# Kernel optimization log

Measured on AMD Instinct MI355X. Metric: run time of the kernel, lower is better.

The kernel has to match this reference:

```python
import jax, jax.numpy as jnp
import numpy as np

VOX_X, VOX_Y, VOX_Z = 256, 256, 20   # ceil((pc_range[3:]-pc_range[:3]) / 0.4)
OUT_H, OUT_W, OUT_Z = 200, 200, 16   # hard-coded F.interpolate target in forward
C = 80                               # out_channels; sparse feat dim must match for concat
N_PTS = 200000
BS = 1
EPS = 1e-5


def _lin_interp(x, axis, out_size):
    """1D linear interp along `axis`, matching torch align_corners=False."""
    in_size = x.shape[axis]
    pos = (jnp.arange(out_size, dtype=jnp.float32) + 0.5) * (in_size / out_size) - 0.5
    pos = jnp.clip(pos, 0.0, in_size - 1)
    i0 = jnp.floor(pos).astype(jnp.int32)
    i1 = jnp.minimum(i0 + 1, in_size - 1)
    w = pos - i0.astype(jnp.float32)
    x0 = jnp.take(x, i0, axis=axis)
    x1 = jnp.take(x, i1, axis=axis)
    wshape = [1] * x.ndim
    wshape[axis] = out_size
    w = w.reshape(wshape)
    return x0 * (1.0 - w) + x1 * w


def setup_inputs() -> dict:
    key = jax.random.key(0)
    ks = jax.random.split(key, 8)
    bev_feats = jax.random.normal(ks[0], (BS, C, OUT_H, OUT_W, OUT_Z), dtype=jnp.float32)
    # coords: [batch_idx, x, y, z] with per-column valid ranges
    cb = jax.random.randint(ks[1], (N_PTS, 1), 0, BS, dtype=jnp.int32)
    cx = jax.random.randint(ks[2], (N_PTS, 1), 0, VOX_X, dtype=jnp.int32)
    cy = jax.random.randint(ks[3], (N_PTS, 1), 0, VOX_Y, dtype=jnp.int32)
    cz = jax.random.randint(ks[4], (N_PTS, 1), 0, VOX_Z, dtype=jnp.int32)
    coords = jnp.concatenate([cb, cx, cy, cz], axis=1)
    feats = jax.random.normal(ks[5], (N_PTS, C), dtype=jnp.float32)
    w_conv = jax.random.normal(ks[6], (C, 2 * C), dtype=jnp.float32) * (1.0 / np.sqrt(2 * C))
    b_conv = jnp.zeros((C,), dtype=jnp.float32)
    return {
        "bev_feats": bev_feats, "coords": coords, "feats": feats,
        "w_conv": w_conv, "b_conv": b_conv,
        "bn_gamma": jnp.ones((C,), jnp.float32), "bn_beta": jnp.zeros((C,), jnp.float32),
        "bn_mean": jnp.zeros((C,), jnp.float32), "bn_var": jnp.ones((C,), jnp.float32),
    }


def reference(bev_feats, coords, feats, w_conv, b_conv, bn_gamma, bn_beta, bn_mean, bn_var):
    bs = bev_feats.shape[0]
    voxel = jnp.zeros((bs, VOX_X, VOX_Y, VOX_Z, C), dtype=jnp.float32)
    voxel = voxel.at[coords[:, 0], coords[:, 1], coords[:, 2], coords[:, 3]].set(feats)
    # permute(0,4,2,1,3): (bs, X, Y, Z, C) -> (bs, C, Y, X, Z)
    prior = jnp.transpose(voxel, (0, 4, 2, 1, 3))
    # trilinear interpolate (256,256,20) -> (200,200,16), align_corners=False (separable)
    prior = _lin_interp(prior, 2, OUT_H)
    prior = _lin_interp(prior, 3, OUT_W)
    prior = _lin_interp(prior, 4, OUT_Z)
    # concat on channels -> 1x1x1 conv3d -> BN (eval stats) -> residual -> ReLU
    x = jnp.concatenate([bev_feats, prior], axis=1)  # (bs, 2C, H, W, Z)
    y = jnp.einsum('bchwz,oc->bohwz', x, w_conv) + b_conv[None, :, None, None, None]
    inv = bn_gamma * jax.lax.rsqrt(bn_var + EPS)
    y = y * inv[None, :, None, None, None] + (bn_beta - bn_mean * inv)[None, :, None, None, None]
    return jax.nn.relu(y + bev_feats)
```

## Files before the change

kernel.cpp:

```cpp
#include <hip/hip_runtime.h>
#include <hip/hip_bf16.h>

#define VXX 256
#define VYY 256
#define VZZ 20
#define NC  80
#define OH  200
#define OW  200
#define OZ  16
#define SPATIAL (OH*OW*OZ)
#define NVOX (VXX*VYY*VZZ)
#define EPSV 1e-5f
#define NS 64
#define RS 168
#define NWG (SPATIAL/NS)
#define X_FOOT 6
#define NCELL (2*X_FOOT*VZZ)
#define SLOTS 48
#define PSTR 72

typedef float  f32x4 __attribute__((ext_vector_type(4)));
typedef short  s16x8 __attribute__((ext_vector_type(8)));

__device__ __forceinline__ ushort f2bf(float f) {
    uint u = __builtin_bit_cast(uint, f);
    u += 0x7FFFu + ((u >> 16) & 1u);
    return (ushort)(u >> 16);
}

__device__ __forceinline__ void bar_lgkm() {
    asm volatile("s_waitcnt lgkmcnt(0)" ::: "memory");
    __builtin_amdgcn_s_barrier();
    asm volatile("" ::: "memory");
}

__global__ void scatter_k(const int* __restrict__ coords, int npts,
                          int* __restrict__ winner) {
    int i = blockIdx.x * 256 + threadIdx.x;
    if (i >= npts) return;
    int b = coords[i*4+0];
    int x = coords[i*4+1];
    int y = coords[i*4+2];
    int z = coords[i*4+3];
    int vi = ((b*VXX + x)*VYY + y)*VZZ + z;
    atomicMax(&winner[vi], i);
}

__global__ void setup_k(const float* __restrict__ wconv,
                        const float* __restrict__ bconv,
                        const float* __restrict__ gamma,
                        const float* __restrict__ beta,
                        const float* __restrict__ mean,
                        const float* __restrict__ var,
                        int4* __restrict__ winner4,
                        ushort* __restrict__ wfrag,
                        float2* __restrict__ bnss) {
    const int b = blockIdx.x, tid = threadIdx.x;
    if (b < 1280) {
        winner4[b*256 + tid] = make_int4(-1, -1, -1, -1);
    } else if (b < 1330) {
        int idx = (b - 1280)*256 + tid;
        int f   = idx >> 9;
        int rem = idx & 511;
        int l   = rem >> 3;
        int j   = rem & 7;
        int mt  = f / 5;
        int ks  = f - mt*5;
        int o   = mt*16 + (l & 15);
        int c   = ks*32 + (l >> 4)*8 + j;
        wfrag[idx] = f2bf(wconv[o*160 + c]);
    } else if (tid < NC) {
        float inv = gamma[tid] * rsqrtf(var[tid] + EPSV);
        bnss[tid] = make_float2(inv, bconv[tid]*inv + beta[tid] - mean[tid]*inv);
    }
}

__launch_bounds__(256, 3)
__global__ void fused_k(const float* __restrict__ bev,
                        const float* __restrict__ feats,
                        const int*  __restrict__ winner,
                        const ushort* __restrict__ wfrag,
                        const float2* __restrict__ bnss,
                        float* __restrict__ out) {
    __shared__ __align__(16) ushort x_lds[NS * RS];
    __shared__ __align__(16) ushort P_lds[NS * PSTR];
    __shared__ __align__(16) ushort Rt_lds[NC * PSTR];
    __shared__ int    idx_lds[NCELL];
    __shared__ int    slot_pi[SLOTS];
    __shared__ int    wavecnt[4];

    const int tid   = threadIdx.x;
    const int bid   = blockIdx.x;
    const int swzb  = (bid & 7) * (NWG/8) + (bid >> 3);
    const int sbase = swzb * NS;
    const int sl    = tid & 63;
    const int quarter = tid >> 6;
    const int wv    = quarter, lane = sl;

    const int h  = sbase / (OW * OZ);
    const int w0 = (sbase >> 4) % OW;
    float posy = (h + 0.5f) * ((float)VYY/(float)OH) - 0.5f;
    posy = fminf(fmaxf(posy, 0.f), (float)(VYY-1));
    const int   y0 = (int)posy;
    const int   y1 = min(y0+1, VYY-1);
    const float fy = posy - (float)y0;
    float posx0 = (w0 + 0.5f) * ((float)VXX/(float)OW) - 0.5f;
    posx0 = fminf(fmaxf(posx0, 0.f), (float)(VXX-1));
    const int xmin = (int)posx0;

    const int zq = sl & 15;
    const int wq = w0 + (sl >> 4);
    float posx = (wq + 0.5f) * ((float)VXX/(float)OW) - 0.5f;
    posx = fminf(fmaxf(posx, 0.f), (float)(VXX-1));
    const int   x0 = (int)posx;
    const int   x1 = min(x0+1, VXX-1);
    const float fxw = posx - (float)x0;
    float posz = (zq + 0.5f) * ((float)VZZ/(float)OZ) - 0.5f;
    posz = fminf(fmaxf(posz, 0.f), (float)(VZZ-1));
    const int   z0 = (int)posz;
    const int   z1 = min(z0+1, VZZ-1);
    const float fzw = posz - (float)z0;
    const int fx0 = x0 - xmin, fx1 = x1 - xmin;

    int pi = -1;
    if (tid < NCELL) {
        int fz  = tid % VZZ;
        int fx  = (tid / VZZ) % X_FOOT;
        int fyc = tid / (VZZ * X_FOOT);
        int xx  = min(xmin + fx, VXX-1);
        int yy  = fyc ? y1 : y0;
        pi = winner[(xx*VYY + yy)*VZZ + fz];
    }
    __builtin_amdgcn_sched_barrier(0);

    const int S = sbase + sl;
    float bvv[20];
    #pragma unroll
    for (int j = 0; j < 20; ++j)
        bvv[j] = bev[(quarter*20 + j)*SPATIAL + S];
    __builtin_amdgcn_sched_barrier(0);

    {
        uint* pz = (uint*)P_lds;
        #pragma unroll
        for (int i = 0; i < 9; ++i) pz[tid + i*256] = 0;
    }

    unsigned long long bm = __ballot(pi >= 0);
    if (lane == 0) wavecnt[wv] = __popcll(bm);
    bar_lgkm();
    int base = 0, nstot = 0;
    #pragma unroll
    for (int w2 = 0; w2 < 4; ++w2) {
        int c2 = wavecnt[w2];
        if (w2 < wv) base += c2;
        nstot += c2;
    }
    if (tid < NCELL) {
        int v = -1;
        if (pi >= 0) {
            int slot = base + __popcll(bm & ((1ull << lane) - 1ull));
            if (slot < SLOTS) { slot_pi[slot] = pi; v = slot; }
            else v = -(pi + 2);
        }
        idx_lds[tid] = v;
    }
    bar_lgkm();
    const int nst = min(nstot, SLOTS);

    const float4* feats4 = (const float4*)feats;
    const int myslot = tid >> 2, part = tid & 3;
    const bool rowact = (myslot < nst);
    float4 rbuf[5];
    if (rowact) {
        const float4* p = feats4 + slot_pi[myslot]*20 + part*5;
        #pragma unroll
        for (int q = 0; q < 5; ++q) rbuf[q] = p[q];
    }

    {
        const int ky = quarter >> 1, kx = quarter & 1;
        const float ywp = ky ? fy : 1.f - fy;
        const bool xdup = (fx1 == fx0);
        if (!(xdup && kx)) {
            const int   xf = kx ? fx1 : fx0;
            const float xw = xdup ? 1.f : (kx ? fxw : 1.f - fxw);
            #pragma unroll
            for (int kz = 0; kz < 2; ++kz) {
                int cell = (ky*X_FOOT + xf)*VZZ + (kz ? z1 : z0);
                int v = idx_lds[cell];
                if (v >= 0)
                    P_lds[sl*PSTR + v] = f2bf(ywp * xw * (kz ? fzw : 1.f - fzw));
            }
        }
    }

    #pragma unroll
    for (int j5 = 0; j5 < 5; ++j5) {
        ushort4 pk = make_ushort4(f2bf(bvv[j5*4+0]), f2bf(bvv[j5*4+1]),
                                  f2bf(bvv[j5*4+2]), f2bf(bvv[j5*4+3]));
        *(ushort4*)&x_lds[sl*RS + quarter*20 + j5*4] = pk;
    }

    {
        ushort vals[20];
        #pragma unroll
        for (int q = 0; q < 5; ++q) {
            vals[4*q+0] = rowact ? f2bf(rbuf[q].x) : (ushort)0;
            vals[4*q+1] = rowact ? f2bf(rbuf[q].y) : (ushort)0;
            vals[4*q+2] = rowact ? f2bf(rbuf[q].z) : (ushort)0;
            vals[4*q+3] = rowact ? f2bf(rbuf[q].w) : (ushort)0;
        }
        #pragma unroll
        for (int e = 0; e < 20; ++e)
            Rt_lds[(part*20 + e)*PSTR + myslot] = vals[e];
    }
    bar_lgkm();

    const int lrow = lane & 15, lgrp = lane >> 4;
    {
        const int prow = (wv*16 + lrow)*PSTR;
        s16x8 p0 = *(const s16x8*)&P_lds[prow +      lgrp*8];
        s16x8 p1 = *(const s16x8*)&P_lds[prow + 32 + lgrp*8];
        #pragma unroll
        for (int mt = 0; mt < 5; ++mt) {
            const int arow = (mt*16 + lrow)*PSTR;
            s16x8 a0 = *(const s16x8*)&Rt_lds[arow +      lgrp*8];
            s16x8 a1 = *(const s16x8*)&Rt_lds[arow + 32 + lgrp*8];
            f32x4 pa = (f32x4){0.f, 0.f, 0.f, 0.f};
            pa = __builtin_amdgcn_mfma_f32_16x16x32_bf16(a0, p0, pa, 0, 0, 0);
            pa = __builtin_amdgcn_mfma_f32_16x16x32_bf16(a1, p1, pa, 0, 0, 0);
            ushort4 pk = make_ushort4(f2bf(pa[0]), f2bf(pa[1]),
                                      f2bf(pa[2]), f2bf(pa[3]));
            *(ushort4*)&x_lds[(wv*16 + lrow)*RS + 80 + mt*16 + lgrp*4] = pk;
        }
    }

    if (nstot > SLOTS) {
        bar_lgkm();
        float add20[20];
        #pragma unroll
        for (int j = 0; j < 20; ++j) add20[j] = 0.f;
        bool any = false;
        #pragma unroll
        for (int k = 0; k < 8; ++k) {
            int kz = k & 1, kx = (k>>1)&1, ky = k>>2;
            int cell = (ky*X_FOOT + (kx ? fx1 : fx0))*VZZ + (kz ? z1 : z0);
            int v = idx_lds[cell];
            if (v < -1) {
                any = true;
                float wtk = (ky?fy:1.f-fy) * (kx?fxw:1.f-fxw) * (kz?fzw:1.f-fzw);
                const float4* p = feats4 + (-v - 2)*20 + quarter*5;
                #pragma unroll
                for (int q = 0; q < 5; ++q) {
                    float4 f = p[q];
                    add20[4*q]   += wtk*f.x; add20[4*q+1] += wtk*f.y;
                    add20[4*q+2] += wtk*f.z; add20[4*q+3] += wtk*f.w;
                }
            }
        }
        if (any) {
            #pragma unroll
            for (int q = 0; q < 5; ++q) {
                ushort* dst = &x_lds[sl*RS + 80 + quarter*20 + q*4];
                ushort4 old = *(ushort4*)dst;
                const ushort ov[4] = {old.x, old.y, old.z, old.w};
                ushort nv[4];
                #pragma unroll
                for (int e = 0; e < 4; ++e) {
                    float f = __builtin_bit_cast(float, (uint)ov[e] << 16) + add20[4*q+e];
                    nv[e] = f2bf(f);
                }
                *(ushort4*)dst = make_ushort4(nv[0], nv[1], nv[2], nv[3]);
            }
        }
    }
    bar_lgkm();

    f32x4 acc[5];
    #pragma unroll
    for (int mt = 0; mt < 5; ++mt) acc[mt] = (f32x4){0.f, 0.f, 0.f, 0.f};

    const int srow = (wv*16 + lrow) * RS;

    #pragma unroll
    for (int ks = 0; ks < 5; ++ks) {
        s16x8 b = *(const s16x8*)&x_lds[srow + ks*32 + lgrp*8];
        #pragma unroll
        for (int mt = 0; mt < 5; ++mt) {
            s16x8 a = *(const s16x8*)&wfrag[((mt*5 + ks)*64 + lane)*8];
            acc[mt] = __builtin_amdgcn_mfma_f32_16x16x32_bf16(a, b, acc[mt], 0, 0, 0);
        }
    }

    const int slocal = wv*16 + lrow;
    const int sglob  = sbase + slocal;
    #pragma unroll
    for (int mt = 0; mt < 5; ++mt) {
        ushort4 rr = *(const ushort4*)&x_lds[slocal*RS + mt*16 + lgrp*4];
        const ushort rrv[4] = {rr.x, rr.y, rr.z, rr.w};
        #pragma unroll
        for (int r = 0; r < 4; ++r) {
            int o = mt*16 + lgrp*4 + r;
            float2 ss = bnss[o];
            float resid = __builtin_bit_cast(float, (uint)rrv[r] << 16);
            float v = acc[mt][r]*ss.x + ss.y + resid;
            out[o*SPATIAL + sglob] = fmaxf(v, 0.f);
        }
    }
}

extern "C" void kernel_launch(void* const* d_in, const int* in_sizes, int n_in,
                              void* d_out, int out_size, void* d_ws, size_t ws_size,
                              hipStream_t stream) {
    const float* bev    = (const float*)d_in[0];
    const int*   coords = (const int*)  d_in[1];
    const float* feats  = (const float*)d_in[2];
    const float* wconv  = (const float*)d_in[3];
    const float* bconv  = (const float*)d_in[4];
    const float* gamma  = (const float*)d_in[5];
    const float* beta   = (const float*)d_in[6];
    const float* mean   = (const float*)d_in[7];
    const float* var    = (const float*)d_in[8];
    float*       out    = (float*)d_out;

    int*    winner = (int*)d_ws;
    ushort* wfrag  = (ushort*)((char*)d_ws + (size_t)NVOX*4);
    float2* bnss   = (float2*)((char*)d_ws + (size_t)NVOX*4 + 25600);
    int npts = in_sizes[1] / 4;

    hipLaunchKernelGGL(setup_k, dim3(1331), dim3(256), 0, stream,
                       wconv, bconv, gamma, beta, mean, var,
                       (int4*)winner, wfrag, bnss);
    hipLaunchKernelGGL(scatter_k, dim3((npts + 255)/256), dim3(256), 0, stream,
                       coords, npts, winner);
    hipLaunchKernelGGL(fused_k, dim3(NWG), dim3(256), 0, stream,
                       bev, feats, winner, wfrag, bnss, out);
}
```

Baseline: 149.5 us.

## Alias P/Rt LDS with prior-feature buffer to cut shared memory, raise occupancy

```diff
diff --git a/kernel.cpp b/kernel.cpp
--- a/kernel.cpp
+++ b/kernel.cpp
@@ -12,12 +12,13 @@
 #define NVOX (VXX*VYY*VZZ)
 #define EPSV 1e-5f
 #define NS 64
-#define RS 168
 #define NWG (SPATIAL/NS)
 #define X_FOOT 6
 #define NCELL (2*X_FOOT*VZZ)
 #define SLOTS 48
 #define PSTR 72
+#define RSB 80
+#define RSP 88
 
 typedef float  f32x4 __attribute__((ext_vector_type(4)));
 typedef short  s16x8 __attribute__((ext_vector_type(8)));
@@ -75,19 +76,21 @@
     }
 }
 
-__launch_bounds__(256, 3)
+__launch_bounds__(256, 5)
 __global__ void fused_k(const float* __restrict__ bev,
                         const float* __restrict__ feats,
                         const int*  __restrict__ winner,
                         const ushort* __restrict__ wfrag,
                         const float2* __restrict__ bnss,
                         float* __restrict__ out) {
-    __shared__ __align__(16) ushort x_lds[NS * RS];
-    __shared__ __align__(16) ushort P_lds[NS * PSTR];
-    __shared__ __align__(16) ushort Rt_lds[NC * PSTR];
+    __shared__ __align__(16) ushort xb_lds[NS * RSB];
+    __shared__ __align__(16) char   u_lds[20736];
     __shared__ int    idx_lds[NCELL];
     __shared__ int    slot_pi[SLOTS];
     __shared__ int    wavecnt[4];
+    ushort* const P_lds  = (ushort*)u_lds;
+    ushort* const Rt_lds = (ushort*)(u_lds + 9216);
+    ushort* const xp_lds = (ushort*)u_lds;
 
     const int tid   = threadIdx.x;
     const int bid   = blockIdx.x;
@@ -141,7 +144,7 @@
     __builtin_amdgcn_sched_barrier(0);
 
     {
-        uint* pz = (uint*)P_lds;
+        uint* pz = (uint*)u_lds;
         #pragma unroll
         for (int i = 0; i < 9; ++i) pz[tid + i*256] = 0;
     }
@@ -199,7 +202,7 @@
     for (int j5 = 0; j5 < 5; ++j5) {
         ushort4 pk = make_ushort4(f2bf(bvv[j5*4+0]), f2bf(bvv[j5*4+1]),
                                   f2bf(bvv[j5*4+2]), f2bf(bvv[j5*4+3]));
-        *(ushort4*)&x_lds[sl*RS + quarter*20 + j5*4] = pk;
+        *(ushort4*)&xb_lds[sl*RSB + quarter*20 + j5*4] = pk;
     }
 
     {
@@ -218,6 +221,7 @@
     bar_lgkm();
 
     const int lrow = lane & 15, lgrp = lane >> 4;
+    f32x4 pa[5];
     {
         const int prow = (wv*16 + lrow)*PSTR;
         s16x8 p0 = *(const s16x8*)&P_lds[prow +      lgrp*8];
@@ -227,13 +231,17 @@
             const int arow = (mt*16 + lrow)*PSTR;
             s16x8 a0 = *(const s16x8*)&Rt_lds[arow +      lgrp*8];
             s16x8 a1 = *(const s16x8*)&Rt_lds[arow + 32 + lgrp*8];
-            f32x4 pa = (f32x4){0.f, 0.f, 0.f, 0.f};
-            pa = __builtin_amdgcn_mfma_f32_16x16x32_bf16(a0, p0, pa, 0, 0, 0);
-            pa = __builtin_amdgcn_mfma_f32_16x16x32_bf16(a1, p1, pa, 0, 0, 0);
-            ushort4 pk = make_ushort4(f2bf(pa[0]), f2bf(pa[1]),
-                                      f2bf(pa[2]), f2bf(pa[3]));
-            *(ushort4*)&x_lds[(wv*16 + lrow)*RS + 80 + mt*16 + lgrp*4] = pk;
-        }
+            pa[mt] = (f32x4){0.f, 0.f, 0.f, 0.f};
+            pa[mt] = __builtin_amdgcn_mfma_f32_16x16x32_bf16(a0, p0, pa[mt], 0, 0, 0);
+            pa[mt] = __builtin_amdgcn_mfma_f32_16x16x32_bf16(a1, p1, pa[mt], 0, 0, 0);
+        }
+    }
+    bar_lgkm();
+    #pragma unroll
+    for (int mt = 0; mt < 5; ++mt) {
+        ushort4 pk = make_ushort4(f2bf(pa[mt][0]), f2bf(pa[mt][1]),
+                                  f2bf(pa[mt][2]), f2bf(pa[mt][3]));
+        *(ushort4*)&xp_lds[(wv*16 + lrow)*RSP + mt*16 + lgrp*4] = pk;
     }
 
     if (nstot > SLOTS) {
@@ -262,7 +270,7 @@
         if (any) {
             #pragma unroll
             for (int q = 0; q < 5; ++q) {
-                ushort* dst = &x_lds[sl*RS + 80 + quarter*20 + q*4];
+                ushort* dst = &xp_lds[sl*RSP + quarter*20 + q*4];
                 ushort4 old = *(ushort4*)dst;
                 const ushort ov[4] = {old.x, old.y, old.z, old.w};
                 ushort nv[4];
@@ -281,11 +289,15 @@
     #pragma unroll
     for (int mt = 0; mt < 5; ++mt) acc[mt] = (f32x4){0.f, 0.f, 0.f, 0.f};
 
-    const int srow = (wv*16 + lrow) * RS;
+    const int srow_b = (wv*16 + lrow) * RSB;
+    const int srow_p = (wv*16 + lrow) * RSP;
 
     #pragma unroll
     for (int ks = 0; ks < 5; ++ks) {
-        s16x8 b = *(const s16x8*)&x_lds[srow + ks*32 + lgrp*8];
+        int c = ks*32 + lgrp*8;
+        const ushort* bp = (c < 80) ? &xb_lds[srow_b + c]
+                                    : &xp_lds[srow_p + (c - 80)];
+        s16x8 b = *(const s16x8*)bp;
         #pragma unroll
         for (int mt = 0; mt < 5; ++mt) {
             s16x8 a = *(const s16x8*)&wfrag[((mt*5 + ks)*64 + lane)*8];
@@ -297,7 +309,7 @@
     const int sglob  = sbase + slocal;
     #pragma unroll
     for (int mt = 0; mt < 5; ++mt) {
-        ushort4 rr = *(const ushort4*)&x_lds[slocal*RS + mt*16 + lgrp*4];
+        ushort4 rr = *(const ushort4*)&xb_lds[slocal*RSB + mt*16 + lgrp*4];
         const ushort rrv[4] = {rr.x, rr.y, rr.z, rr.w};
         #pragma unroll
         for (int r = 0; r < 4; ++r) {
```

After: 151.2 us. Within noise of the previous version (+1.2%).
